# Optimization experiments

Hardware: AMD Instinct MI355X
Metric: run time of the kernel (lower is better)

Reference implementation:

```python
import jax, jax.numpy as jnp
import numpy as np

B, N, L, C = 16, 2048, 12, 32  # batch, num_nodes, seq_len, channels


def setup_inputs() -> dict:
    key = jax.random.key(0)
    k1, k2, k3 = jax.random.split(key, 3)
    x = jax.random.normal(k1, (B, N, L, C), dtype=jnp.float32)
    # memory parameter: xavier_uniform over (channels, num_nodes)
    limit = float(np.sqrt(6.0 / (C + N)))
    memory = jax.random.uniform(k2, (C, N), minval=-limit, maxval=limit, dtype=jnp.float32)
    # nn.Linear(2, 1): weight (1, 2), bias (1,)
    fc_limit = float(np.sqrt(1.0 / 2.0))
    fc_w = jax.random.uniform(k3, (1, 2), minval=-fc_limit, maxval=fc_limit, dtype=jnp.float32)
    fc_b = jnp.zeros((1,), dtype=jnp.float32)
    return {"x": x, "memory": memory, "fc_w": fc_w, "fc_b": fc_b}


def reference(x, memory, fc_w, fc_b):
    # x: (B, N, L, C) -> permute to (B, C, N, L) as in the torch module
    xp = jnp.transpose(x, (0, 3, 1, 2))
    scale = 1.0 / float(np.sqrt(xp.shape[1]))  # 1/sqrt(channels)
    # adj_dyn_1: einsum over channel+time with memory -> (B, N, N)
    a1 = jax.nn.softmax(jax.nn.relu(jnp.einsum('bcnl,cm->bnm', xp, memory) * scale), axis=-1)
    # adj_dyn_2: time-summed node features gram matrix -> (B, N, N)
    xs = xp.sum(-1)  # (B, C, N)
    a2 = jax.nn.softmax(jax.nn.relu(jnp.einsum('bcn,bcm->bnm', xs, xs) * scale), axis=-1)
    # fc over the stacked pair: Linear(2,1) == w0*a1 + w1*a2 + b
    adj = a1 * fc_w[0, 0] + a2 * fc_w[0, 1] + fc_b[0]  # (B, N, N)
    k = int(adj.shape[1] * 0.8)
    _, idx = jax.lax.top_k(adj, k)  # idx: (B, N, k)
    b_ix = jnp.arange(adj.shape[0])[:, None, None]
    n_ix = jnp.arange(adj.shape[1])[None, :, None]
    mask = jnp.zeros_like(adj).at[b_ix, n_ix, idx].set(1.0)
    return jax.nn.softmax(adj * mask, axis=-1)
```

## Files before the change

### kernel.cpp

```cpp
#include <hip/hip_runtime.h>
#include <hip/hip_bf16.h>
#include <cstdint>
#include <cstddef>

#define B_ 16
#define N_ 2048
#define L_ 12
#define C_ 32
#define KTOP 1638
#define SCALE 0.17677669529663687f
#define LOG2E 1.44269504088896f

typedef __attribute__((ext_vector_type(8))) short short8v;
typedef __attribute__((ext_vector_type(4))) float f32x4;

#if __has_builtin(__builtin_amdgcn_exp2f)
#define EXP2F(x) __builtin_amdgcn_exp2f(x)
#else
#define EXP2F(x) exp2f(x)
#endif

__device__ __forceinline__ unsigned short bf16_rne(float v) {
  unsigned u = __float_as_uint(v);
  u += 0x7FFFu + ((u >> 16) & 1u);
  return (unsigned short)(u >> 16);
}
__device__ __forceinline__ unsigned key15(unsigned short b16) {
  const unsigned s = b16 >> 15;
  return ((((unsigned)b16) ^ 0x8000u ^ (s * 0x7FFFu)) >> 1) & 0x7FFFu;
}

__global__ __launch_bounds__(256) void prep_kernel(const float* __restrict__ x,
                                                   const float* __restrict__ mem,
                                                   unsigned short* __restrict__ xsH,
                                                   unsigned short* __restrict__ xsL,
                                                   unsigned short* __restrict__ memT) {
  const int b = blockIdx.y, n0 = blockIdx.x * 64;
  const int c = threadIdx.x & 31, nr = threadIdx.x >> 5;
#pragma unroll
  for (int i = 0; i < 8; ++i) {
    const int n = n0 + i * 8 + nr;
    const float* px = x + ((size_t)(b * N_ + n) * L_) * C_ + c;
    float s = 0.f;
#pragma unroll
    for (int l = 0; l < L_; ++l) s += px[l * C_];
    const unsigned short h = bf16_rne(s);
    const float hf = __uint_as_float((unsigned)h << 16);
    const unsigned short lo = bf16_rne(s - hf);
    const size_t o = (size_t)(b * N_ + n) * C_ + c;
    xsH[o] = h;
    xsL[o] = lo;
  }
  if (b == 0) {
#pragma unroll
    for (int i = 0; i < 8; ++i) {
      const int idx = i * 256 + threadIdx.x;
      const int ml = idx >> 5, cc = idx & 31;
      memT[(size_t)(n0 + ml) * C_ + cc] = bf16_rne(mem[(size_t)cc * N_ + n0 + ml]);
    }
  }
}

__global__ __launch_bounds__(512, 6) void adj_kernel(
    const unsigned short* __restrict__ xsH, const unsigned short* __restrict__ xsL,
    const unsigned short* __restrict__ memT, const float* __restrict__ fc_w,
    const float* __restrict__ fc_b, float* __restrict__ out) {
  __shared__ unsigned char  p1b[8][2080];
  __shared__ unsigned short p2b[8][2064];
  __shared__ float red1[8][8], red2[8][8];

  const int tid = threadIdx.x, wid = tid >> 6, lane = tid & 63;
  const int l15 = lane & 15, g = lane >> 4;
  const int b = blockIdx.y, n0 = blockIdx.x * 8;

  const int fr = (l15 < 8) ? l15 : ((l15 - 6) & 7);
  const int rbase = (g & 1) * 4 + (g & 2);
  const int g8 = g * 8;
  const size_t arow = (size_t)(b * N_ + n0 + fr) * C_ + g8;
  const short8v hiA = *(const short8v*)(xsH + arow);
  const short8v loFA = *(const short8v*)(xsL + arow);

  const f32x4 zero = {0.f, 0.f, 0.f, 0.f};
  const float K = SCALE * LOG2E;
  const float C2 = -80.f * LOG2E;
  const int mbase = wid * 256 + l15;
  const size_t bcol = (size_t)b * N_ * C_ + (size_t)mbase * C_ + g8;
  const unsigned short* pH = xsH + bcol;
  const unsigned short* pL = xsL + bcol;
  const unsigned short* pM = memT + (size_t)mbase * C_ + g8;

  float s1[2] = {0.f, 0.f}, s2[2] = {0.f, 0.f};

#pragma unroll 2
  for (int t = 0; t < 16; ++t) {
    const short8v hiB = *(const short8v*)(pH + t * (16 * C_));
    const short8v loB = *(const short8v*)(pL + t * (16 * C_));
    const short8v mB  = *(const short8v*)(pM + t * (16 * C_));

    f32x4 acc1 = __builtin_amdgcn_mfma_f32_16x16x32_bf16(hiA, mB, zero, 0, 0, 0);
    f32x4 acc2 = __builtin_amdgcn_mfma_f32_16x16x32_bf16(hiA, hiB, zero, 0, 0, 0);
    acc2 = __builtin_amdgcn_mfma_f32_16x16x32_bf16(hiA, loB, acc2, 0, 0, 0);
    acc2 = __builtin_amdgcn_mfma_f32_16x16x32_bf16(loFA, hiB, acc2, 0, 0, 0);

    const int m = mbase + t * 16;
#pragma unroll
    for (int s = 0; s < 2; ++s) {
      const float p1 = EXP2F(fmaxf(acc1[s], 0.f) * K);
      const float p2 = EXP2F(fminf(fmaf(fmaxf(acc2[s], 0.f), K, C2), 127.f));
      s1[s] += p1; s2[s] += p2;
      p1b[rbase + s][m] = (unsigned char)fminf(fmaf(p1, 128.f, -127.5f), 255.f);
      p2b[rbase + s][m] = bf16_rne(p2);
    }
  }

#pragma unroll
  for (int d = 1; d < 16; d <<= 1) {
#pragma unroll
    for (int s = 0; s < 2; ++s) {
      s1[s] += __shfl_xor(s1[s], d);
      s2[s] += __shfl_xor(s2[s], d);
    }
  }
  if (l15 == 0) {
#pragma unroll
    for (int s = 0; s < 2; ++s) {
      red1[wid][rbase + s] = s1[s];
      red2[wid][rbase + s] = s2[s];
    }
  }
  __syncthreads();

  const int r = wid;
  float S1 = 0.f, S2 = 0.f;
#pragma unroll
  for (int w = 0; w < 8; ++w) { S1 += red1[w][r]; S2 += red2[w][r]; }
  const float w0 = fc_w[0], w1 = fc_w[1], bb = fc_b[0];
  const float i1 = w0 / S1, i2 = w1 / S2;

  unsigned pk[16], kg[16];
  const unsigned char*  pr1 = &p1b[r][0];
  const unsigned short* pr2 = &p2b[r][0];
#pragma unroll
  for (int k = 0; k < 8; ++k) {
    const int c0 = 4 * lane + 256 * k;
    const unsigned q8 = *(const unsigned*)(pr1 + c0);
    const ushort4 q16 = *(const ushort4*)(pr2 + c0);
    const float a0 = fmaf(__uint_as_float((unsigned)q16.x << 16), i2,
                    fmaf(fmaf((float)(unsigned char)(q8      ), 0.0078125f, 1.f), i1, bb));
    const float a1 = fmaf(__uint_as_float((unsigned)q16.y << 16), i2,
                    fmaf(fmaf((float)(unsigned char)(q8 >>  8), 0.0078125f, 1.f), i1, bb));
    const float a2 = fmaf(__uint_as_float((unsigned)q16.z << 16), i2,
                    fmaf(fmaf((float)(unsigned char)(q8 >> 16), 0.0078125f, 1.f), i1, bb));
    const float a3 = fmaf(__uint_as_float((unsigned)q16.w << 16), i2,
                    fmaf(fmaf((float)(unsigned char)(q8 >> 24), 0.0078125f, 1.f), i1, bb));
    union { __hip_bfloat162 h2; unsigned u; } cA, cB;
    cA.h2 = __float22bfloat162_rn(float2{a0, a1});
    cB.h2 = __float22bfloat162_rn(float2{a2, a3});
    pk[2 * k] = cA.u; pk[2 * k + 1] = cB.u;
    unsigned sgn = (cA.u >> 15) & 0x00010001u;
    unsigned srt = cA.u ^ 0x80008000u ^ (sgn * 0x7FFFu);
    kg[2 * k] = ((srt >> 1) & 0x7FFF7FFFu) | 0x80008000u;
    sgn = (cB.u >> 15) & 0x00010001u;
    srt = cB.u ^ 0x80008000u ^ (sgn * 0x7FFFu);
    kg[2 * k + 1] = ((srt >> 1) & 0x7FFF7FFFu) | 0x80008000u;
  }

  const float p2t = __uint_as_float((unsigned)bf16_rne(EXP2F(C2)) << 16);
  const unsigned kT = key15(bf16_rne(fmaf(p2t, i2, fmaf(1.0f, i1, bb))));
  const unsigned mmA = kT * 0x10001u;
  const unsigned mmB = (kT + 1u) * 0x10001u;
  unsigned cge = 0, cgt = 0;
#pragma unroll
  for (int j = 0; j < 16; ++j) {
    cge += ((kg[j] - mmA) >> 15) & 0x10001u;
    cgt += ((kg[j] - mmB) >> 15) & 0x10001u;
  }
  unsigned comb = ((cge & 0xFFFFu) + (cge >> 16)) |
                  (((cgt & 0xFFFFu) + (cgt >> 16)) << 16);
#pragma unroll
  for (int d = 1; d < 64; d <<= 1) comb += (unsigned)__shfl_xor((int)comb, d);
  const unsigned nge = comb & 0xFFFFu, ngt = comb >> 16;
  unsigned thr = kT;
  if (!(nge >= KTOP && ngt < KTOP)) {
    unsigned mn = 0x7FFFu, mx = 0u;
#pragma unroll
    for (int j = 0; j < 16; ++j) {
      const unsigned k15 = kg[j] & 0x7FFF7FFFu;
      mn = min(mn, min(k15 & 0xFFFFu, k15 >> 16));
      mx = max(mx, max(k15 & 0xFFFFu, k15 >> 16));
    }
#pragma unroll
    for (int d = 1; d < 64; d <<= 1) {
      mn = min(mn, (unsigned)__shfl_xor((int)mn, d));
      mx = max(mx, (unsigned)__shfl_xor((int)mx, d));
    }
    unsigned lo2, hi2;
    if (nge < KTOP) { lo2 = mn; hi2 = kT - 1u; } else { lo2 = kT + 1u; hi2 = mx; }
#pragma unroll 1
    for (int it = 0; it < 15; ++it) {
      if (lo2 >= hi2) break;
      const unsigned mid = (lo2 + hi2 + 1u) >> 1;
      const unsigned mm = mid * 0x10001u;
      unsigned c0 = 0;
#pragma unroll
      for (int j = 0; j < 16; ++j) c0 += ((kg[j] - mm) >> 15) & 0x10001u;
      unsigned cnt = (c0 & 0xFFFFu) + (c0 >> 16);
#pragma unroll
      for (int d = 1; d < 64; d <<= 1) cnt += (unsigned)__shfl_xor((int)cnt, d);
      if (cnt >= KTOP) lo2 = mid; else hi2 = mid - 1u;
    }
    thr = lo2;
  }

  const unsigned lolo = thr * 0x10001u;
  float ssum = 0.f;
#pragma unroll
  for (int j = 0; j < 16; ++j) {
    const unsigned ge = kg[j] - lolo;
    const unsigned msk = ((ge & 0x8000u) ? 0xFFFFu : 0u) |
                         ((ge & 0x80000000u) ? 0xFFFF0000u : 0u);
    pk[j] &= msk;
    const float aA = __uint_as_float(pk[j] << 16);
    const float aB = __uint_as_float(pk[j] & 0xFFFF0000u);
    float eA = fmaf(aA, fmaf(aA, fmaf(aA, 0.166666667f, 0.5f), 1.f), 1.f);
    float eB = fmaf(aB, fmaf(aB, fmaf(aB, 0.166666667f, 0.5f), 1.f), 1.f);
    if (__ballot(fmaxf(__builtin_fabsf(aA), __builtin_fabsf(aB)) > 0.25f)) {
      eA = EXP2F(aA * LOG2E);
      eB = EXP2F(aB * LOG2E);
    }
    ssum += eA + eB;
  }
#pragma unroll
  for (int d = 1; d < 64; d <<= 1) ssum += __shfl_xor(ssum, d);
  const float inv = 1.f / ssum;

  float* op = out + ((size_t)(b * N_ + n0 + r)) * N_;
#pragma unroll
  for (int k = 0; k < 8; ++k) {
    float e4[4];
#pragma unroll
    for (int h = 0; h < 2; ++h) {
      const unsigned pj = pk[2 * k + h];
      const float aA = __uint_as_float(pj << 16);
      const float aB = __uint_as_float(pj & 0xFFFF0000u);
      float eA = fmaf(aA, fmaf(aA, fmaf(aA, 0.166666667f, 0.5f), 1.f), 1.f);
      float eB = fmaf(aB, fmaf(aB, fmaf(aB, 0.166666667f, 0.5f), 1.f), 1.f);
      if (__ballot(fmaxf(__builtin_fabsf(aA), __builtin_fabsf(aB)) > 0.25f)) {
        eA = EXP2F(aA * LOG2E);
        eB = EXP2F(aB * LOG2E);
      }
      e4[2 * h] = eA; e4[2 * h + 1] = eB;
    }
    float4 o;
    o.x = e4[0] * inv; o.y = e4[1] * inv; o.z = e4[2] * inv; o.w = e4[3] * inv;
    *(float4*)(op + 4 * lane + 256 * k) = o;
  }
}

extern "C" void kernel_launch(void* const* d_in, const int* in_sizes, int n_in,
                              void* d_out, int out_size, void* d_ws, size_t ws_size,
                              hipStream_t stream) {
  const float* x   = (const float*)d_in[0];
  const float* mem = (const float*)d_in[1];
  const float* fcw = (const float*)d_in[2];
  const float* fcb = (const float*)d_in[3];
  float* out = (float*)d_out;
  unsigned short* xsH  = (unsigned short*)d_ws;
  unsigned short* xsL  = xsH + (size_t)B_ * N_ * C_;
  unsigned short* memT = xsL + (size_t)B_ * N_ * C_;

  dim3 g1(N_ / 64, B_);
  prep_kernel<<<g1, 256, 0, stream>>>(x, mem, xsH, xsL, memT);
  dim3 g2(N_ / 8, B_);
  adj_kernel<<<g2, 512, 0, stream>>>(xsH, xsL, memT, fcw, fcb, out);
}
```

Baseline: 161.6 us.

## Add fast-path threshold check in fp32 with fused exp and packed bf16 LDS buffer

Packs p1 and p2 as a bf16 pair into one 32-bit LDS word per element, replacing the separate 8-bit and bf16 buffers. The common case, where the analytic threshold already selects exactly KTOP elements, is now handled in a single pass that counts, masks, evaluates a degree-4 exp polynomial and sums, storing exponentials as bf16 for output. The binary-search path becomes a separate slow path that recomputes from LDS. The main loop is fully unrolled and the occupancy hint drops from 6 to 4, which adds register pressure and bf16 rounding of outputs in the fast path.

```diff
diff --git a/kernel.cpp b/kernel.cpp
--- a/kernel.cpp
+++ b/kernel.cpp
@@ -29,6 +29,9 @@
   const unsigned s = b16 >> 15;
   return ((((unsigned)b16) ^ 0x8000u ^ (s * 0x7FFFu)) >> 1) & 0x7FFFu;
 }
+__device__ __forceinline__ float exp_poly4(float x) {
+  return fmaf(x, fmaf(x, fmaf(x, fmaf(x, 0.041666667f, 0.166666667f), 0.5f), 1.f), 1.f);
+}
 
 __global__ __launch_bounds__(256) void prep_kernel(const float* __restrict__ x,
                                                    const float* __restrict__ mem,
@@ -61,12 +64,11 @@
   }
 }
 
-__global__ __launch_bounds__(512, 6) void adj_kernel(
+__global__ __launch_bounds__(512, 4) void adj_kernel(
     const unsigned short* __restrict__ xsH, const unsigned short* __restrict__ xsL,
     const unsigned short* __restrict__ memT, const float* __restrict__ fc_w,
     const float* __restrict__ fc_b, float* __restrict__ out) {
-  __shared__ unsigned char  p1b[8][2080];
-  __shared__ unsigned short p2b[8][2064];
+  __shared__ unsigned pbuf[8][2049];
   __shared__ float red1[8][8], red2[8][8];
 
   const int tid = threadIdx.x, wid = tid >> 6, lane = tid & 63;
@@ -88,10 +90,11 @@
   const unsigned short* pH = xsH + bcol;
   const unsigned short* pL = xsL + bcol;
   const unsigned short* pM = memT + (size_t)mbase * C_ + g8;
+  unsigned* pw = &pbuf[rbase][mbase];
 
   float s1[2] = {0.f, 0.f}, s2[2] = {0.f, 0.f};
 
-#pragma unroll 2
+#pragma unroll
   for (int t = 0; t < 16; ++t) {
     const short8v hiB = *(const short8v*)(pH + t * (16 * C_));
     const short8v loB = *(const short8v*)(pL + t * (16 * C_));
@@ -102,14 +105,14 @@
     acc2 = __builtin_amdgcn_mfma_f32_16x16x32_bf16(hiA, loB, acc2, 0, 0, 0);
     acc2 = __builtin_amdgcn_mfma_f32_16x16x32_bf16(loFA, hiB, acc2, 0, 0, 0);
 
-    const int m = mbase + t * 16;
 #pragma unroll
     for (int s = 0; s < 2; ++s) {
       const float p1 = EXP2F(fmaxf(acc1[s], 0.f) * K);
       const float p2 = EXP2F(fminf(fmaf(fmaxf(acc2[s], 0.f), K, C2), 127.f));
       s1[s] += p1; s2[s] += p2;
-      p1b[rbase + s][m] = (unsigned char)fminf(fmaf(p1, 128.f, -127.5f), 255.f);
-      p2b[rbase + s][m] = bf16_rne(p2);
+      union { __hip_bfloat162 h2; unsigned u; } pk;
+      pk.h2 = __float22bfloat162_rn(float2{p1, p2});
+      pw[s * 2049 + t * 16] = pk.u;
     }
   }
 
@@ -136,52 +139,81 @@
   for (int w = 0; w < 8; ++w) { S1 += red1[w][r]; S2 += red2[w][r]; }
   const float w0 = fc_w[0], w1 = fc_w[1], bb = fc_b[0];
   const float i1 = w0 / S1, i2 = w1 / S2;
-
-  unsigned pk[16], kg[16];
-  const unsigned char*  pr1 = &p1b[r][0];
-  const unsigned short* pr2 = &p2b[r][0];
+  const unsigned* prow = &pbuf[0][0] + r * 2049;
+
+  const float p2t = __uint_as_float((unsigned)bf16_rne(EXP2F(C2)) << 16);
+  const float T = fmaf(p2t, i2, fmaf(1.0f, i1, bb));
+
+  unsigned exb[16];
+  float ssum = 0.f;
+  unsigned cge = 0, cgt = 0;
 #pragma unroll
   for (int k = 0; k < 8; ++k) {
-    const int c0 = 4 * lane + 256 * k;
-    const unsigned q8 = *(const unsigned*)(pr1 + c0);
-    const ushort4 q16 = *(const ushort4*)(pr2 + c0);
-    const float a0 = fmaf(__uint_as_float((unsigned)q16.x << 16), i2,
-                    fmaf(fmaf((float)(unsigned char)(q8      ), 0.0078125f, 1.f), i1, bb));
-    const float a1 = fmaf(__uint_as_float((unsigned)q16.y << 16), i2,
-                    fmaf(fmaf((float)(unsigned char)(q8 >>  8), 0.0078125f, 1.f), i1, bb));
-    const float a2 = fmaf(__uint_as_float((unsigned)q16.z << 16), i2,
-                    fmaf(fmaf((float)(unsigned char)(q8 >> 16), 0.0078125f, 1.f), i1, bb));
-    const float a3 = fmaf(__uint_as_float((unsigned)q16.w << 16), i2,
-                    fmaf(fmaf((float)(unsigned char)(q8 >> 24), 0.0078125f, 1.f), i1, bb));
-    union { __hip_bfloat162 h2; unsigned u; } cA, cB;
-    cA.h2 = __float22bfloat162_rn(float2{a0, a1});
-    cB.h2 = __float22bfloat162_rn(float2{a2, a3});
-    pk[2 * k] = cA.u; pk[2 * k + 1] = cB.u;
-    unsigned sgn = (cA.u >> 15) & 0x00010001u;
-    unsigned srt = cA.u ^ 0x80008000u ^ (sgn * 0x7FFFu);
-    kg[2 * k] = ((srt >> 1) & 0x7FFF7FFFu) | 0x80008000u;
-    sgn = (cB.u >> 15) & 0x00010001u;
-    srt = cB.u ^ 0x80008000u ^ (sgn * 0x7FFFu);
-    kg[2 * k + 1] = ((srt >> 1) & 0x7FFF7FFFu) | 0x80008000u;
-  }
-
-  const float p2t = __uint_as_float((unsigned)bf16_rne(EXP2F(C2)) << 16);
-  const unsigned kT = key15(bf16_rne(fmaf(p2t, i2, fmaf(1.0f, i1, bb))));
-  const unsigned mmA = kT * 0x10001u;
-  const unsigned mmB = (kT + 1u) * 0x10001u;
-  unsigned cge = 0, cgt = 0;
-#pragma unroll
-  for (int j = 0; j < 16; ++j) {
-    cge += ((kg[j] - mmA) >> 15) & 0x10001u;
-    cgt += ((kg[j] - mmB) >> 15) & 0x10001u;
-  }
-  unsigned comb = ((cge & 0xFFFFu) + (cge >> 16)) |
-                  (((cgt & 0xFFFFu) + (cgt >> 16)) << 16);
-#pragma unroll
-  for (int d = 1; d < 64; d <<= 1) comb += (unsigned)__shfl_xor((int)comb, d);
-  const unsigned nge = comb & 0xFFFFu, ngt = comb >> 16;
-  unsigned thr = kT;
-  if (!(nge >= KTOP && ngt < KTOP)) {
+    const uint4 q = *(const uint4*)&prow[4 * lane + 256 * k];
+    const unsigned qq[4] = {q.x, q.y, q.z, q.w};
+    float e4[4];
+#pragma unroll
+    for (int c4 = 0; c4 < 4; ++c4) {
+      const float p1 = __uint_as_float(qq[c4] << 16);
+      const float p2 = __uint_as_float(qq[c4] & 0xFFFF0000u);
+      const float adj = fmaf(p2, i2, fmaf(p1, i1, bb));
+      cge += (adj >= T) ? 1u : 0u;
+      cgt += (adj >  T) ? 1u : 0u;
+      const float am = (adj >= T) ? adj : 0.f;
+      const float e = exp_poly4(am);
+      e4[c4] = e;
+      ssum += e;
+    }
+    union { __hip_bfloat162 h2; unsigned u; } pa, pb2;
+    pa.h2  = __float22bfloat162_rn(float2{e4[0], e4[1]});
+    pb2.h2 = __float22bfloat162_rn(float2{e4[2], e4[3]});
+    exb[2 * k] = pa.u; exb[2 * k + 1] = pb2.u;
+  }
+  unsigned comb = cge | (cgt << 16);
+#pragma unroll
+  for (int d = 1; d < 64; d <<= 1) {
+    comb += (unsigned)__shfl_xor((int)comb, d);
+    ssum += __shfl_xor(ssum, d);
+  }
+  const unsigned CGE = comb & 0xFFFFu, CGT = comb >> 16;
+
+  float* op = out + ((size_t)(b * N_ + n0 + r)) * N_;
+
+  if (CGE >= KTOP && CGT < KTOP) {
+    const float inv = 1.f / ssum;
+#pragma unroll
+    for (int k = 0; k < 8; ++k) {
+      float4 o;
+      o.x = __uint_as_float(exb[2 * k] << 16) * inv;
+      o.y = __uint_as_float(exb[2 * k] & 0xFFFF0000u) * inv;
+      o.z = __uint_as_float(exb[2 * k + 1] << 16) * inv;
+      o.w = __uint_as_float(exb[2 * k + 1] & 0xFFFF0000u) * inv;
+      *(float4*)(op + 4 * lane + 256 * k) = o;
+    }
+  } else {
+    unsigned pk2[16], kg[16];
+#pragma unroll
+    for (int k = 0; k < 8; ++k) {
+      const uint4 q = *(const uint4*)&prow[4 * lane + 256 * k];
+      const unsigned qq[4] = {q.x, q.y, q.z, q.w};
+      float a4[4];
+#pragma unroll
+      for (int c4 = 0; c4 < 4; ++c4) {
+        const float p1 = __uint_as_float(qq[c4] << 16);
+        const float p2 = __uint_as_float(qq[c4] & 0xFFFF0000u);
+        a4[c4] = fmaf(p2, i2, fmaf(p1, i1, bb));
+      }
+      union { __hip_bfloat162 h2; unsigned u; } cA, cB;
+      cA.h2 = __float22bfloat162_rn(float2{a4[0], a4[1]});
+      cB.h2 = __float22bfloat162_rn(float2{a4[2], a4[3]});
+      pk2[2 * k] = cA.u; pk2[2 * k + 1] = cB.u;
+      unsigned sgn = (cA.u >> 15) & 0x00010001u;
+      unsigned srt = cA.u ^ 0x80008000u ^ (sgn * 0x7FFFu);
+      kg[2 * k] = ((srt >> 1) & 0x7FFF7FFFu) | 0x80008000u;
+      sgn = (pk2[2 * k + 1] >> 15) & 0x00010001u;
+      srt = pk2[2 * k + 1] ^ 0x80008000u ^ (sgn * 0x7FFFu);
+      kg[2 * k + 1] = ((srt >> 1) & 0x7FFF7FFFu) | 0x80008000u;
+    }
     unsigned mn = 0x7FFFu, mx = 0u;
 #pragma unroll
     for (int j = 0; j < 16; ++j) {
@@ -194,8 +226,7 @@
       mn = min(mn, (unsigned)__shfl_xor((int)mn, d));
       mx = max(mx, (unsigned)__shfl_xor((int)mx, d));
     }
-    unsigned lo2, hi2;
-    if (nge < KTOP) { lo2 = mn; hi2 = kT - 1u; } else { lo2 = kT + 1u; hi2 = mx; }
+    unsigned lo2 = mn, hi2 = mx;
 #pragma unroll 1
     for (int it = 0; it < 15; ++it) {
       if (lo2 >= hi2) break;
@@ -209,51 +240,29 @@
       for (int d = 1; d < 64; d <<= 1) cnt += (unsigned)__shfl_xor((int)cnt, d);
       if (cnt >= KTOP) lo2 = mid; else hi2 = mid - 1u;
     }
-    thr = lo2;
-  }
-
-  const unsigned lolo = thr * 0x10001u;
-  float ssum = 0.f;
-#pragma unroll
-  for (int j = 0; j < 16; ++j) {
-    const unsigned ge = kg[j] - lolo;
-    const unsigned msk = ((ge & 0x8000u) ? 0xFFFFu : 0u) |
-                         ((ge & 0x80000000u) ? 0xFFFF0000u : 0u);
-    pk[j] &= msk;
-    const float aA = __uint_as_float(pk[j] << 16);
-    const float aB = __uint_as_float(pk[j] & 0xFFFF0000u);
-    float eA = fmaf(aA, fmaf(aA, fmaf(aA, 0.166666667f, 0.5f), 1.f), 1.f);
-    float eB = fmaf(aB, fmaf(aB, fmaf(aB, 0.166666667f, 0.5f), 1.f), 1.f);
-    if (__ballot(fmaxf(__builtin_fabsf(aA), __builtin_fabsf(aB)) > 0.25f)) {
-      eA = EXP2F(aA * LOG2E);
-      eB = EXP2F(aB * LOG2E);
-    }
-    ssum += eA + eB;
-  }
-#pragma unroll
-  for (int d = 1; d < 64; d <<= 1) ssum += __shfl_xor(ssum, d);
-  const float inv = 1.f / ssum;
-
-  float* op = out + ((size_t)(b * N_ + n0 + r)) * N_;
-#pragma unroll
-  for (int k = 0; k < 8; ++k) {
-    float e4[4];
-#pragma unroll
-    for (int h = 0; h < 2; ++h) {
-      const unsigned pj = pk[2 * k + h];
-      const float aA = __uint_as_float(pj << 16);
-      const float aB = __uint_as_float(pj & 0xFFFF0000u);
-      float eA = fmaf(aA, fmaf(aA, fmaf(aA, 0.166666667f, 0.5f), 1.f), 1.f);
-      float eB = fmaf(aB, fmaf(aB, fmaf(aB, 0.166666667f, 0.5f), 1.f), 1.f);
-      if (__ballot(fmaxf(__builtin_fabsf(aA), __builtin_fabsf(aB)) > 0.25f)) {
-        eA = EXP2F(aA * LOG2E);
-        eB = EXP2F(aB * LOG2E);
-      }
-      e4[2 * h] = eA; e4[2 * h + 1] = eB;
-    }
-    float4 o;
-    o.x = e4[0] * inv; o.y = e4[1] * inv; o.z = e4[2] * inv; o.w = e4[3] * inv;
-    *(float4*)(op + 4 * lane + 256 * k) = o;
+    const unsigned lolo = lo2 * 0x10001u;
+    float s2sum = 0.f;
+    float exf[32];
+#pragma unroll
+    for (int j = 0; j < 16; ++j) {
+      const unsigned ge = kg[j] - lolo;
+      const float aA = (ge & 0x8000u) ? __uint_as_float(pk2[j] << 16) : 0.f;
+      const float aB = (ge & 0x80000000u) ? __uint_as_float(pk2[j] & 0xFFFF0000u) : 0.f;
+      const float eA = EXP2F(aA * LOG2E);
+      const float eB = EXP2F(aB * LOG2E);
+      exf[2 * j] = eA; exf[2 * j + 1] = eB;
+      s2sum += eA + eB;
+    }
+#pragma unroll
+    for (int d = 1; d < 64; d <<= 1) s2sum += __shfl_xor(s2sum, d);
+    const float inv = 1.f / s2sum;
+#pragma unroll
+    for (int k = 0; k < 8; ++k) {
+      float4 o;
+      o.x = exf[4 * k + 0] * inv; o.y = exf[4 * k + 1] * inv;
+      o.z = exf[4 * k + 2] * inv; o.w = exf[4 * k + 3] * inv;
+      *(float4*)(op + 4 * lane + 256 * k) = o;
+    }
   }
 }
 
```

New measurement: 133.3 us. 17.5% less time.
